# Optimization experiments

Hardware: AMD Instinct MI355X
Metric: run time of the kernel (lower is better)

Reference implementation:

```python
import jax, jax.numpy as jnp
import numpy as np

S = 4096      # seq_len
D = 1024      # d_model
H = 16        # n_heads
E = 64        # head dim (D // H)
SCALE0 = 1.0 / np.sqrt(E)  # sh_scale_factor


def setup_inputs() -> dict:
    key = jax.random.key(0)
    ks = jax.random.split(key, 10)
    std = 1.0 / np.sqrt(D)
    inputs = jax.random.normal(ks[0], (S, D), dtype=jnp.float32)
    # per-head projection weights stacked over heads: [H, D, E]
    Wq = jax.random.normal(ks[1], (H, D, E), dtype=jnp.float32) * std
    bq = jnp.zeros((H, E), dtype=jnp.float32)
    Wk = jax.random.normal(ks[2], (H, D, E), dtype=jnp.float32) * std
    bk = jnp.zeros((H, E), dtype=jnp.float32)
    Wv = jax.random.normal(ks[3], (H, D, E), dtype=jnp.float32) * std
    bv = jnp.zeros((H, E), dtype=jnp.float32)
    # learned per-head scalar scale, initialized to 1/sqrt(E)
    scale = jnp.full((H,), SCALE0, dtype=jnp.float32)
    # output projection (stored as [D_in, D_out])
    Wo = jax.random.normal(ks[4], (H * E, D), dtype=jnp.float32) * std
    bo = jnp.zeros((D,), dtype=jnp.float32)
    return {"inputs": inputs, "Wq": Wq, "bq": bq, "Wk": Wk, "bk": bk,
            "Wv": Wv, "bv": bv, "scale": scale, "Wo": Wo, "bo": bo}


def reference(inputs, Wq, bq, Wk, bk, Wv, bv, scale, Wo, bo):
    # per-head QKV projections, batched over heads: [H, S, E]
    q = jnp.einsum('sd,hde->hse', inputs, Wq) + bq[:, None, :]
    k = jnp.einsum('sd,hde->hse', inputs, Wk) + bk[:, None, :]
    v = jnp.einsum('sd,hde->hse', inputs, Wv) + bv[:, None, :]
    # scores [H, S, S], learned scalar scale per head, softmax over keys
    scores = jnp.einsum('hqe,hke->hqk', q, k) * scale[:, None, None]
    attn = jax.nn.softmax(scores, axis=-1)
    o = jnp.einsum('hqk,hke->hqe', attn, v)           # [H, S, E]
    o = jnp.transpose(o, (1, 0, 2)).reshape(S, H * E)  # concat heads on dim 1
    return o @ Wo + bo                                 # [S, D]
```

## Files before the change

kernel.cpp:

```cpp
#include <hip/hip_runtime.h>
#include <stdint.h>

#define S_LEN 4096
#define D_MOD 1024
#define NH    16
#define EH    64

typedef short bf16x8 __attribute__((ext_vector_type(8)));
typedef float f32x4  __attribute__((ext_vector_type(4)));
typedef float f32x16 __attribute__((ext_vector_type(16)));

__device__ __forceinline__ unsigned short f2b(float x){
    uint32_t u = __float_as_uint(x);
    u = (u + 0x7fffu + ((u >> 16) & 1u)) >> 16;
    return (unsigned short)u;
}

__device__ __forceinline__ uint32_t cvtpk_bf16(float lo, float hi){
    uint32_t r;
    asm volatile("v_cvt_pk_bf16_f32 %0, %1, %2" : "=v"(r) : "v"(lo), "v"(hi));
    return r;
}

__device__ __forceinline__ void gld_lds16(const void* g, void* l){
    __builtin_amdgcn_global_load_lds((const __attribute__((address_space(1))) void*)g,
                                     (__attribute__((address_space(3))) void*)l, 16, 0, 0);
}

#define PSWAP_U(a, b) asm volatile("v_permlane32_swap_b32 %0, %1" : "+v"(a), "+v"(b))

#define WAITV8() asm volatile("s_waitcnt vmcnt(8)" ::: "memory")
#define WAITV0() asm volatile("s_waitcnt vmcnt(0)" ::: "memory")
#define CFENCE() asm volatile("" ::: "memory")


__global__ void k_conv_x(const float* __restrict__ x, unsigned short* __restrict__ xb, int n){
    int i = (blockIdx.x * blockDim.x + threadIdx.x) * 4;
    if (i < n){
        float4 v = *(const float4*)(x + i);
        ushort4 o;
        o.x = f2b(v.x); o.y = f2b(v.y); o.z = f2b(v.z); o.w = f2b(v.w);
        *(ushort4*)(xb + i) = o;
    }
}

__global__ void k_conv_w(const float* __restrict__ Wq, const float* __restrict__ Wk,
                         const float* __restrict__ Wv, unsigned short* __restrict__ wt){
    __shared__ float lt[64][65];
    const int tid = threadIdx.x;
    const int d0 = blockIdx.x * 64;
    const int th = blockIdx.y;
    const int t = th >> 4, h = th & 15;
    const float* W = (t == 0) ? Wq : ((t == 1) ? Wk : Wv);
    #pragma unroll
    for (int i = 0; i < 16; i++){
        int idx = tid + 256 * i;
        int dl = idx >> 6, e = idx & 63;
        lt[dl][e] = W[((size_t)((h << 10) + d0 + dl) << 6) + e];
    }
    __syncthreads();
    #pragma unroll
    for (int i = 0; i < 16; i++){
        int idx = tid + 256 * i;
        int eo = idx >> 6, dlo = idx & 63;
        wt[((size_t)((t << 10) + (h << 6) + eo) << 10) + d0 + dlo] = f2b(lt[dlo][eo]);
    }
}

__global__ void k_conv_wo(const float* __restrict__ Wo, unsigned short* __restrict__ wot){
    __shared__ float lt[64][65];
    const int tid = threadIdx.x;
    const int he0 = blockIdx.x * 64, d0 = blockIdx.y * 64;
    #pragma unroll
    for (int i = 0; i < 16; i++){
        int idx = tid + 256 * i;
        int r = idx >> 6, c = idx & 63;
        lt[r][c] = Wo[((size_t)(he0 + r) << 10) + d0 + c];
    }
    __syncthreads();
    #pragma unroll
    for (int i = 0; i < 16; i++){
        int idx = tid + 256 * i;
        int rr = idx >> 6, cc = idx & 63;
        wot[((size_t)(d0 + rr) << 10) + he0 + cc] = f2b(lt[cc][rr]);
    }
}


template<int MODE, int NI>
__global__ __launch_bounds__(256, 4)
void k_gemm(const unsigned short* __restrict__ A, const unsigned short* __restrict__ B, int K,
            unsigned short* __restrict__ qb, unsigned short* __restrict__ kb,
            unsigned short* __restrict__ vb,
            const float* __restrict__ b0, const float* __restrict__ b1, const float* __restrict__ b2,
            const float* __restrict__ scl,
            float* __restrict__ outp, const float* __restrict__ bo){
    __shared__ uint4 lsA4[1024];
    __shared__ uint4 lsB4[NI * 256];
    char* lsA = (char*)lsA4;
    char* lsB = (char*)lsB4;
    const int tid = threadIdx.x;
    const int lane = tid & 63, w = tid >> 6;
    const int lr = lane & 15, lg = lane >> 4;
    const int wm = w >> 1, wn = w & 1;
    const int m0 = blockIdx.y * 128, n0 = blockIdx.x * (32 * NI);
    const int wbase = tid & ~63;

    f32x4 acc[4][NI] = {};

    for (int k0 = 0; k0 < K; k0 += 64){
        __syncthreads();
        #pragma unroll
        for (int i = 0; i < 4; i++){
            int s = tid + 256 * i;
            int row = s >> 3, c = s & 7;
            int cs = c ^ (row & 7);
            gld_lds16(A + (size_t)(m0 + row) * K + k0 + cs * 8, lsA + (wbase + 256 * i) * 16);
        }
        #pragma unroll
        for (int i = 0; i < NI; i++){
            int s = tid + 256 * i;
            int row = s >> 3, c = s & 7;
            int cs = c ^ (row & 7);
            gld_lds16(B + (size_t)(n0 + row) * K + k0 + cs * 8, lsB + (wbase + 256 * i) * 16);
        }
        __syncthreads();
        #pragma unroll
        for (int kc = 0; kc < 2; kc++){
            bf16x8 af[4], bf[NI];
            #pragma unroll
            for (int mi = 0; mi < 4; mi++){
                int row = wm * 64 + mi * 16 + lr;
                int j = kc * 4 + lg;
                af[mi] = *(const bf16x8*)(lsA + row * 128 + (j ^ (row & 7)) * 16);
            }
            #pragma unroll
            for (int ni = 0; ni < NI; ni++){
                int row = wn * (NI * 16) + ni * 16 + lr;
                int j = kc * 4 + lg;
                bf[ni] = *(const bf16x8*)(lsB + row * 128 + (j ^ (row & 7)) * 16);
            }
            #pragma unroll
            for (int mi = 0; mi < 4; mi++)
                #pragma unroll
                for (int ni = 0; ni < NI; ni++)
                    acc[mi][ni] = __builtin_amdgcn_mfma_f32_16x16x32_bf16(af[mi], bf[ni], acc[mi][ni], 0, 0, 0);
        }
    }

    #pragma unroll
    for (int mi = 0; mi < 4; mi++){
        #pragma unroll
        for (int ni = 0; ni < NI; ni++){
            int gnb = n0 + wn * (NI * 16) + ni * 16;
            if (MODE == 0){
                int t = gnb >> 10, h = (gnb >> 6) & 15;
                int e = (gnb & 63) + lr;
                const float* bp = (t == 0) ? b0 : ((t == 1) ? b1 : b2);
                float badd = bp[(h << 6) + e];
                float qs = (t == 0) ? scl[h] * 1.4426950408889634f : 1.0f;
                #pragma unroll
                for (int r = 0; r < 4; r++){
                    int gm = m0 + wm * 64 + mi * 16 + lg * 4 + r;
                    if (t == 0)       qb[((size_t)((h << 12) + gm) << 6) + e] = f2b((acc[mi][ni][r] + badd) * qs);
                    else if (t == 1)  kb[((size_t)((h << 12) + gm) << 6) + e] = f2b(acc[mi][ni][r] + badd);
                    else              vb[(size_t)((h << 6) + e) * 4096 + gm] = f2b(acc[mi][ni][r] + badd);
                }
            } else {
                int gn = gnb + lr;
                float badd = bo[gn];
                #pragma unroll
                for (int r = 0; r < 4; r++){
                    int gm = m0 + wm * 64 + mi * 16 + lg * 4 + r;
                    outp[(size_t)gm * 1024 + gn] = acc[mi][ni][r] + badd;
                }
            }
        }
    }
}


__global__ __launch_bounds__(256, 2)
void k_attn(const unsigned short* __restrict__ qb, const unsigned short* __restrict__ kb,
            const unsigned short* __restrict__ vb, unsigned short* __restrict__ ob){
    __shared__ uint4 ldsb[4096];
    char* ldsc = (char*)ldsb;

    const int tid = threadIdx.x;
    const int lane = tid & 63, w = tid >> 6;
    const int ql = lane & 31, hi = lane >> 5;

    int wg = blockIdx.y * 32 + blockIdx.x;
    wg = (wg & 7) * 64 + (wg >> 3);
    const int h = wg >> 5;
    const int q0 = (wg & 31) * 128 + w * 32;

    bf16x8 qf[4];
    #pragma unroll
    for (int kc = 0; kc < 4; kc++)
        qf[kc] = *(const bf16x8*)(qb + (size_t)((h << 12) + q0 + ql) * 64 + kc * 16 + hi * 8);

    bf16x8 ones;
    #pragma unroll
    for (int j = 0; j < 8; j++) ones[j] = (short)0x3F80;

    f32x16 oA[2] = {}, oB[2] = {}, lacc = {};

    const int et_s = w >> 1;
    const int ksb_s = (w & 1) * 64;

    auto stage = [&](int buf, int kt){
        char* Kd = ldsc + buf * 32768;
        char* Vd = Kd + 16384;
        const unsigned short* ksrc = kb + ((size_t)(h << 12) + kt + w * 32 + ql) * 64 + hi * 8;
        const unsigned short* vsrc = vb + (size_t)((h << 6) + et_s * 32 + ql) * 4096 + kt + ksb_s + hi * 8;
        #pragma unroll
        for (int c = 0; c < 4; c++){
            gld_lds16(ksrc + c * 16, Kd + (w * 256 + c * 64) * 16);
            gld_lds16(vsrc + c * 16, Vd + (w * 256 + c * 64) * 16);
        }
    };

    stage(0, 0);
    stage(1, 128);

    int buf = 0;
    for (int t = 0; t < 32; t++){
        if (t < 31) WAITV8();
        else        WAITV0();
        __builtin_amdgcn_s_barrier();
        CFENCE();

        const char* Kc = ldsc + buf * 32768;
        const char* Vc = Kc + 16384;

        f32x16 s[4];
        __builtin_amdgcn_s_setprio(1);
        #pragma unroll
        for (int kt2 = 0; kt2 < 4; kt2++){
            f32x16 sx = {};
            #pragma unroll
            for (int kc = 0; kc < 4; kc++){
                bf16x8 kf = *(const bf16x8*)(Kc + kt2 * 4096 + kc * 1024 + lane * 16);
                sx = __builtin_amdgcn_mfma_f32_32x32x16_bf16(kf, qf[kc], sx, 0, 0, 0);
            }
            s[kt2] = sx;
        }
        __builtin_amdgcn_s_setprio(0);

        bf16x8 pa[8];
        #pragma unroll
        for (int kt2 = 0; kt2 < 4; kt2++){
            #pragma unroll
            for (int r = 0; r < 16; r++)
                s[kt2][r] = __builtin_amdgcn_exp2f(s[kt2][r]);
            uint32_t a0 = cvtpk_bf16(s[kt2][0], s[kt2][1]);
            uint32_t a1 = cvtpk_bf16(s[kt2][2], s[kt2][3]);
            uint32_t b0 = cvtpk_bf16(s[kt2][4], s[kt2][5]);
            uint32_t b1 = cvtpk_bf16(s[kt2][6], s[kt2][7]);
            PSWAP_U(a0, b0);
            PSWAP_U(a1, b1);
            uint32_t f0[4] = {a0, a1, b0, b1};
            pa[kt2 * 2 + 0] = *(bf16x8*)f0;
            uint32_t c0 = cvtpk_bf16(s[kt2][8],  s[kt2][9]);
            uint32_t c1 = cvtpk_bf16(s[kt2][10], s[kt2][11]);
            uint32_t d0 = cvtpk_bf16(s[kt2][12], s[kt2][13]);
            uint32_t d1 = cvtpk_bf16(s[kt2][14], s[kt2][15]);
            PSWAP_U(c0, d0);
            PSWAP_U(c1, d1);
            uint32_t f1[4] = {c0, c1, d0, d1};
            pa[kt2 * 2 + 1] = *(bf16x8*)f1;
        }

        __builtin_amdgcn_s_setprio(1);
        #pragma unroll
        for (int et = 0; et < 2; et++){
            #pragma unroll
            for (int ks = 0; ks < 4; ks++){
                bf16x8 vfA = *(const bf16x8*)(Vc + et * 8192 + ks * 1024 + lane * 16);
                oA[et] = __builtin_amdgcn_mfma_f32_32x32x16_bf16(vfA, pa[ks], oA[et], 0, 0, 0);
                bf16x8 vfB = *(const bf16x8*)(Vc + et * 8192 + (ks + 4) * 1024 + lane * 16);
                oB[et] = __builtin_amdgcn_mfma_f32_32x32x16_bf16(vfB, pa[ks + 4], oB[et], 0, 0, 0);
            }
        }
        #pragma unroll
        for (int ks = 0; ks < 8; ks++)
            lacc = __builtin_amdgcn_mfma_f32_32x32x16_bf16(ones, pa[ks], lacc, 0, 0, 0);
        __builtin_amdgcn_s_setprio(0);
        CFENCE();

        if (t + 2 < 32){
            __builtin_amdgcn_s_barrier();
            CFENCE();
            stage(buf, (t + 2) * 128);
        }
        buf ^= 1;
    }

    float inv = 1.0f / lacc[0];
    #pragma unroll
    for (int et = 0; et < 2; et++){
        f32x16 o = oA[et] + oB[et];
        #pragma unroll
        for (int g = 0; g < 4; g++){
            ushort4 o4;
            o4.x = f2b(o[4 * g + 0] * inv);
            o4.y = f2b(o[4 * g + 1] * inv);
            o4.z = f2b(o[4 * g + 2] * inv);
            o4.w = f2b(o[4 * g + 3] * inv);
            int e = et * 32 + 8 * g + 4 * hi;
            *(ushort4*)(ob + (size_t)(q0 + ql) * 1024 + (h << 6) + e) = o4;
        }
    }
}


extern "C" void kernel_launch(void* const* d_in, const int* in_sizes, int n_in,
                              void* d_out, int out_size, void* d_ws, size_t ws_size,
                              hipStream_t stream){
    const float* x  = (const float*)d_in[0];
    const float* Wq = (const float*)d_in[1];
    const float* bq = (const float*)d_in[2];
    const float* Wk = (const float*)d_in[3];
    const float* bk = (const float*)d_in[4];
    const float* Wv = (const float*)d_in[5];
    const float* bv = (const float*)d_in[6];
    const float* sc = (const float*)d_in[7];
    const float* Wo = (const float*)d_in[8];
    const float* bo = (const float*)d_in[9];
    float* out = (float*)d_out;
    char* ws = (char*)d_ws;
    const size_t MB = 1u << 20;

    unsigned short* xb  = (unsigned short*)(ws + 0);
    unsigned short* ob  = xb;
    unsigned short* wt  = (unsigned short*)(ws + 8  * MB);
    unsigned short* wot = (unsigned short*)(ws + 14 * MB);
    unsigned short* qb  = (unsigned short*)(ws + 16 * MB);
    unsigned short* kb  = (unsigned short*)(ws + 24 * MB);
    unsigned short* vb  = (unsigned short*)(ws + 32 * MB);

    k_conv_x <<<4096, 256, 0, stream>>>(x, xb, S_LEN * D_MOD);
    k_conv_w <<<dim3(16, 48), 256, 0, stream>>>(Wq, Wk, Wv, wt);
    k_conv_wo<<<dim3(16, 16), 256, 0, stream>>>(Wo, wot);

    k_gemm<0, 4><<<dim3(24, 32), 256, 0, stream>>>(xb, wt, D_MOD, qb, kb, vb, bq, bk, bv, sc, nullptr, nullptr);
    k_attn      <<<dim3(32, 16), 256, 0, stream>>>(qb, kb, vb, ob);
    k_gemm<1, 2><<<dim3(16, 32), 256, 0, stream>>>(ob, wot, D_MOD, nullptr, nullptr, nullptr,
                                                   nullptr, nullptr, nullptr, nullptr, out, bo);
}
```

Measured before the change: 169.4 us.

## Software-pipeline QK^T of next tile with softmax of current; compute row sum on VALU

Restructures the attention loop so the QK^T MFMAs for tile t+1 are issued interleaved with the exp/pack work for tile t, using two score register sets and a 2x unrolled loop. K and V staging are split so the K buffer can be refilled earlier than V. The row-sum is now accumulated with scalar adds plus a permlane swap instead of eight extra MFMAs against a ones vector. This aims to overlap transcendental VALU work with matrix-core work and drop redundant MFMAs, at the cost of more registers (extra f32x16 arrays) and a more delicate wait/barrier schedule.

```diff
diff --git a/kernel.cpp b/kernel.cpp
--- a/kernel.cpp
+++ b/kernel.cpp
@@ -29,7 +29,19 @@
 
 #define PSWAP_U(a, b) asm volatile("v_permlane32_swap_b32 %0, %1" : "+v"(a), "+v"(b))
 
+__device__ __forceinline__ float vcopy(float x){
+    float y;
+    asm volatile("v_mov_b32 %0, %1" : "=v"(y) : "v"(x));
+    return y;
+}
+__device__ __forceinline__ float pswap_add(float x){
+    uint32_t a = __float_as_uint(x), b = __float_as_uint(vcopy(x));
+    PSWAP_U(a, b);
+    return __uint_as_float(a) + __uint_as_float(b);
+}
+
 #define WAITV8() asm volatile("s_waitcnt vmcnt(8)" ::: "memory")
+#define WAITV4() asm volatile("s_waitcnt vmcnt(4)" ::: "memory")
 #define WAITV0() asm volatile("s_waitcnt vmcnt(0)" ::: "memory")
 #define CFENCE() asm volatile("" ::: "memory")
 
@@ -200,77 +212,103 @@
     for (int kc = 0; kc < 4; kc++)
         qf[kc] = *(const bf16x8*)(qb + (size_t)((h << 12) + q0 + ql) * 64 + kc * 16 + hi * 8);
 
-    bf16x8 ones;
-    #pragma unroll
-    for (int j = 0; j < 8; j++) ones[j] = (short)0x3F80;
-
-    f32x16 oA[2] = {}, oB[2] = {}, lacc = {};
+    f32x16 oA[2] = {}, oB[2] = {};
+    float l_run = 0.f;
 
     const int et_s = w >> 1;
     const int ksb_s = (w & 1) * 64;
 
-    auto stage = [&](int buf, int kt){
-        char* Kd = ldsc + buf * 32768;
-        char* Vd = Kd + 16384;
+    auto stage_K = [&](int b, int kt){
+        char* Kd = ldsc + b * 32768;
         const unsigned short* ksrc = kb + ((size_t)(h << 12) + kt + w * 32 + ql) * 64 + hi * 8;
+        #pragma unroll
+        for (int c = 0; c < 4; c++)
+            gld_lds16(ksrc + c * 16, Kd + (w * 256 + c * 64) * 16);
+    };
+    auto stage_V = [&](int b, int kt){
+        char* Vd = ldsc + b * 32768 + 16384;
         const unsigned short* vsrc = vb + (size_t)((h << 6) + et_s * 32 + ql) * 4096 + kt + ksb_s + hi * 8;
         #pragma unroll
-        for (int c = 0; c < 4; c++){
-            gld_lds16(ksrc + c * 16, Kd + (w * 256 + c * 64) * 16);
+        for (int c = 0; c < 4; c++)
             gld_lds16(vsrc + c * 16, Vd + (w * 256 + c * 64) * 16);
-        }
     };
 
-    stage(0, 0);
-    stage(1, 128);
-
-    int buf = 0;
-    for (int t = 0; t < 32; t++){
-        if (t < 31) WAITV8();
-        else        WAITV0();
-        __builtin_amdgcn_s_barrier();
-        CFENCE();
-
-        const char* Kc = ldsc + buf * 32768;
-        const char* Vc = Kc + 16384;
-
-        f32x16 s[4];
-        __builtin_amdgcn_s_setprio(1);
-        #pragma unroll
-        for (int kt2 = 0; kt2 < 4; kt2++){
-            f32x16 sx = {};
-            #pragma unroll
-            for (int kc = 0; kc < 4; kc++){
-                bf16x8 kf = *(const bf16x8*)(Kc + kt2 * 4096 + kc * 1024 + lane * 16);
-                sx = __builtin_amdgcn_mfma_f32_32x32x16_bf16(kf, qf[kc], sx, 0, 0, 0);
-            }
-            s[kt2] = sx;
-        }
-        __builtin_amdgcn_s_setprio(0);
-
+    auto smpack = [&](f32x16& v, bf16x8& p0, bf16x8& p1, float& psum){
+        #pragma unroll
+        for (int r = 0; r < 16; r++){
+            v[r] = __builtin_amdgcn_exp2f(v[r]);
+            psum += v[r];
+        }
+        uint32_t a0 = cvtpk_bf16(v[0], v[1]);
+        uint32_t a1 = cvtpk_bf16(v[2], v[3]);
+        uint32_t b0 = cvtpk_bf16(v[4], v[5]);
+        uint32_t b1 = cvtpk_bf16(v[6], v[7]);
+        PSWAP_U(a0, b0);
+        PSWAP_U(a1, b1);
+        uint32_t f0[4] = {a0, a1, b0, b1};
+        p0 = *(bf16x8*)f0;
+        uint32_t c0 = cvtpk_bf16(v[8],  v[9]);
+        uint32_t c1 = cvtpk_bf16(v[10], v[11]);
+        uint32_t d0 = cvtpk_bf16(v[12], v[13]);
+        uint32_t d1 = cvtpk_bf16(v[14], v[15]);
+        PSWAP_U(c0, d0);
+        PSWAP_U(c1, d1);
+        uint32_t f1[4] = {c0, c1, d0, d1};
+        p1 = *(bf16x8*)f1;
+    };
+
+    stage_K(0, 0);   stage_V(0, 0);
+    stage_K(1, 128); stage_V(1, 128);
+    WAITV8();
+    __builtin_amdgcn_s_barrier();
+    CFENCE();
+
+    f32x16 sA[4], sB[4];
+    __builtin_amdgcn_s_setprio(1);
+    #pragma unroll
+    for (int kt2 = 0; kt2 < 4; kt2++){
+        f32x16 sx = {};
+        #pragma unroll
+        for (int kc = 0; kc < 4; kc++){
+            bf16x8 kf = *(const bf16x8*)(ldsc + kt2 * 4096 + kc * 1024 + lane * 16);
+            sx = __builtin_amdgcn_mfma_f32_32x32x16_bf16(kf, qf[kc], sx, 0, 0, 0);
+        }
+        sA[kt2] = sx;
+    }
+    __builtin_amdgcn_s_setprio(0);
+
+    auto body = [&](f32x16 (&cur)[4], f32x16 (&nxt)[4], int t){
+        const int bi = t & 1;
+        const char* Kn = ldsc + (bi ^ 1) * 32768;
+        const char* Vc = ldsc + bi * 32768 + 16384;
         bf16x8 pa[8];
-        #pragma unroll
-        for (int kt2 = 0; kt2 < 4; kt2++){
-            #pragma unroll
-            for (int r = 0; r < 16; r++)
-                s[kt2][r] = __builtin_amdgcn_exp2f(s[kt2][r]);
-            uint32_t a0 = cvtpk_bf16(s[kt2][0], s[kt2][1]);
-            uint32_t a1 = cvtpk_bf16(s[kt2][2], s[kt2][3]);
-            uint32_t b0 = cvtpk_bf16(s[kt2][4], s[kt2][5]);
-            uint32_t b1 = cvtpk_bf16(s[kt2][6], s[kt2][7]);
-            PSWAP_U(a0, b0);
-            PSWAP_U(a1, b1);
-            uint32_t f0[4] = {a0, a1, b0, b1};
-            pa[kt2 * 2 + 0] = *(bf16x8*)f0;
-            uint32_t c0 = cvtpk_bf16(s[kt2][8],  s[kt2][9]);
-            uint32_t c1 = cvtpk_bf16(s[kt2][10], s[kt2][11]);
-            uint32_t d0 = cvtpk_bf16(s[kt2][12], s[kt2][13]);
-            uint32_t d1 = cvtpk_bf16(s[kt2][14], s[kt2][15]);
-            PSWAP_U(c0, d0);
-            PSWAP_U(c1, d1);
-            uint32_t f1[4] = {c0, c1, d0, d1};
-            pa[kt2 * 2 + 1] = *(bf16x8*)f1;
-        }
+        float psum = 0.f;
+
+        if (t < 31){
+            WAITV4();
+            __builtin_amdgcn_s_barrier();
+            CFENCE();
+            if (t + 2 < 32) stage_K(bi, (t + 2) * 128);
+            #pragma unroll
+            for (int kt2 = 0; kt2 < 4; kt2++){
+                f32x16 sx = {};
+                #pragma unroll
+                for (int kc = 0; kc < 4; kc++){
+                    bf16x8 kf = *(const bf16x8*)(Kn + kt2 * 4096 + kc * 1024 + lane * 16);
+                    sx = __builtin_amdgcn_mfma_f32_32x32x16_bf16(kf, qf[kc], sx, 0, 0, 0);
+                }
+                nxt[kt2] = sx;
+                smpack(cur[kt2], pa[kt2 * 2], pa[kt2 * 2 + 1], psum);
+            }
+        } else {
+            WAITV0();
+            __builtin_amdgcn_s_barrier();
+            CFENCE();
+            #pragma unroll
+            for (int kt2 = 0; kt2 < 4; kt2++)
+                smpack(cur[kt2], pa[kt2 * 2], pa[kt2 * 2 + 1], psum);
+        }
+        l_run += psum;
 
         __builtin_amdgcn_s_setprio(1);
         #pragma unroll
@@ -283,21 +321,24 @@
                 oB[et] = __builtin_amdgcn_mfma_f32_32x32x16_bf16(vfB, pa[ks + 4], oB[et], 0, 0, 0);
             }
         }
-        #pragma unroll
-        for (int ks = 0; ks < 8; ks++)
-            lacc = __builtin_amdgcn_mfma_f32_32x32x16_bf16(ones, pa[ks], lacc, 0, 0, 0);
         __builtin_amdgcn_s_setprio(0);
         CFENCE();
 
         if (t + 2 < 32){
             __builtin_amdgcn_s_barrier();
             CFENCE();
-            stage(buf, (t + 2) * 128);
-        }
-        buf ^= 1;
-    }
-
-    float inv = 1.0f / lacc[0];
+            stage_V(bi, (t + 2) * 128);
+        }
+    };
+
+    #pragma unroll 1
+    for (int t = 0; t < 32; t += 2){
+        body(sA, sB, t);
+        body(sB, sA, t + 1);
+    }
+
+    float l = pswap_add(l_run);
+    float inv = 1.0f / l;
     #pragma unroll
     for (int et = 0; et < 2; et++){
         f32x16 o = oA[et] + oB[et];
```

After: 256.7 us. 1.52x slower.

## Replace ones-MFMA row-sum with VALU accumulation and interleave exp with PV MFMAs

Applied to the files above, without the earlier changes.

Drops the eight extra MFMAs per tile that multiplied P by a ones vector to get the softmax denominator. The sum is now accumulated in fp32 on the VALU while exponentials are computed, and the two half-waves are combined with a permlane32 swap at the end. It also interleaves the PV MFMAs with the exp and convert work per sub-tile rather than running them in a separate phase, removing the pa[] register array. The intent is to cut matrix-core work and let VALU and MFMA overlap. Two things differ from before: the denominator is now summed from the unrounded fp32 exponentials rather than the bf16-rounded P, and the setprio hints around the PV phase are removed.

```diff
diff --git a/kernel.cpp b/kernel.cpp
--- a/kernel.cpp
+++ b/kernel.cpp
@@ -28,6 +28,17 @@
 }
 
 #define PSWAP_U(a, b) asm volatile("v_permlane32_swap_b32 %0, %1" : "+v"(a), "+v"(b))
+
+__device__ __forceinline__ float vcopy(float x){
+    float y;
+    asm volatile("v_mov_b32 %0, %1" : "=v"(y) : "v"(x));
+    return y;
+}
+__device__ __forceinline__ float pswap_add(float x){
+    uint32_t a = __float_as_uint(x), b = __float_as_uint(vcopy(x));
+    PSWAP_U(a, b);
+    return __uint_as_float(a) + __uint_as_float(b);
+}
 
 #define WAITV8() asm volatile("s_waitcnt vmcnt(8)" ::: "memory")
 #define WAITV0() asm volatile("s_waitcnt vmcnt(0)" ::: "memory")
@@ -200,11 +211,8 @@
     for (int kc = 0; kc < 4; kc++)
         qf[kc] = *(const bf16x8*)(qb + (size_t)((h << 12) + q0 + ql) * 64 + kc * 16 + hi * 8);
 
-    bf16x8 ones;
-    #pragma unroll
-    for (int j = 0; j < 8; j++) ones[j] = (short)0x3F80;
-
-    f32x16 oA[2] = {}, oB[2] = {}, lacc = {};
+    f32x16 oA[2] = {}, oB[2] = {};
+    float l_run = 0.f;
 
     const int et_s = w >> 1;
     const int ksb_s = (w & 1) * 64;
@@ -248,45 +256,39 @@
         }
         __builtin_amdgcn_s_setprio(0);
 
-        bf16x8 pa[8];
         #pragma unroll
         for (int kt2 = 0; kt2 < 4; kt2++){
-            #pragma unroll
-            for (int r = 0; r < 16; r++)
-                s[kt2][r] = __builtin_amdgcn_exp2f(s[kt2][r]);
-            uint32_t a0 = cvtpk_bf16(s[kt2][0], s[kt2][1]);
-            uint32_t a1 = cvtpk_bf16(s[kt2][2], s[kt2][3]);
-            uint32_t b0 = cvtpk_bf16(s[kt2][4], s[kt2][5]);
-            uint32_t b1 = cvtpk_bf16(s[kt2][6], s[kt2][7]);
+            f32x16& v = s[kt2];
+            #pragma unroll
+            for (int r = 0; r < 16; r++){
+                v[r] = __builtin_amdgcn_exp2f(v[r]);
+                l_run += v[r];
+            }
+            uint32_t a0 = cvtpk_bf16(v[0], v[1]);
+            uint32_t a1 = cvtpk_bf16(v[2], v[3]);
+            uint32_t b0 = cvtpk_bf16(v[4], v[5]);
+            uint32_t b1 = cvtpk_bf16(v[6], v[7]);
             PSWAP_U(a0, b0);
             PSWAP_U(a1, b1);
             uint32_t f0[4] = {a0, a1, b0, b1};
-            pa[kt2 * 2 + 0] = *(bf16x8*)f0;
-            uint32_t c0 = cvtpk_bf16(s[kt2][8],  s[kt2][9]);
-            uint32_t c1 = cvtpk_bf16(s[kt2][10], s[kt2][11]);
-            uint32_t d0 = cvtpk_bf16(s[kt2][12], s[kt2][13]);
-            uint32_t d1 = cvtpk_bf16(s[kt2][14], s[kt2][15]);
+            bf16x8 p0 = *(bf16x8*)f0;
+            uint32_t c0 = cvtpk_bf16(v[8],  v[9]);
+            uint32_t c1 = cvtpk_bf16(v[10], v[11]);
+            uint32_t d0 = cvtpk_bf16(v[12], v[13]);
+            uint32_t d1 = cvtpk_bf16(v[14], v[15]);
             PSWAP_U(c0, d0);
             PSWAP_U(c1, d1);
             uint32_t f1[4] = {c0, c1, d0, d1};
-            pa[kt2 * 2 + 1] = *(bf16x8*)f1;
-        }
-
-        __builtin_amdgcn_s_setprio(1);
-        #pragma unroll
-        for (int et = 0; et < 2; et++){
-            #pragma unroll
-            for (int ks = 0; ks < 4; ks++){
-                bf16x8 vfA = *(const bf16x8*)(Vc + et * 8192 + ks * 1024 + lane * 16);
-                oA[et] = __builtin_amdgcn_mfma_f32_32x32x16_bf16(vfA, pa[ks], oA[et], 0, 0, 0);
-                bf16x8 vfB = *(const bf16x8*)(Vc + et * 8192 + (ks + 4) * 1024 + lane * 16);
-                oB[et] = __builtin_amdgcn_mfma_f32_32x32x16_bf16(vfB, pa[ks + 4], oB[et], 0, 0, 0);
-            }
-        }
-        #pragma unroll
-        for (int ks = 0; ks < 8; ks++)
-            lacc = __builtin_amdgcn_mfma_f32_32x32x16_bf16(ones, pa[ks], lacc, 0, 0, 0);
-        __builtin_amdgcn_s_setprio(0);
+            bf16x8 p1 = *(bf16x8*)f1;
+
+            #pragma unroll
+            for (int et = 0; et < 2; et++){
+                bf16x8 vf0 = *(const bf16x8*)(Vc + et * 8192 + (2 * kt2) * 1024 + lane * 16);
+                oA[et] = __builtin_amdgcn_mfma_f32_32x32x16_bf16(vf0, p0, oA[et], 0, 0, 0);
+                bf16x8 vf1 = *(const bf16x8*)(Vc + et * 8192 + (2 * kt2 + 1) * 1024 + lane * 16);
+                oB[et] = __builtin_amdgcn_mfma_f32_32x32x16_bf16(vf1, p1, oB[et], 0, 0, 0);
+            }
+        }
         CFENCE();
 
         if (t + 2 < 32){
@@ -297,7 +299,8 @@
         buf ^= 1;
     }
 
-    float inv = 1.0f / lacc[0];
+    float l = pswap_add(l_run);
+    float inv = 1.0f / l;
     #pragma unroll
     for (int et = 0; et < 2; et++){
         f32x16 o = oA[et] + oB[et];
```

New measurement: 164.4 us. 3.0% less time.
